# Kernel optimization log

Measured on AMD Instinct MI355X. Metric: run time of the kernel, lower is better.

## Reference

```python
import jax, jax.numpy as jnp
import numpy as np
from jax import lax

B, L, H = 2, 1024, 1024
D = 2048          # intermediate_size
N = 16            # ssm state size
K = 4             # conv kernel
R = 64            # time_step_rank


def setup_inputs() -> dict:
    key = jax.random.key(0)
    ks = jax.random.split(key, 10)
    def nrm(k, shape, scale=0.02):
        return jax.random.normal(k, shape, dtype=jnp.float32) * scale
    A = jnp.arange(1, N + 1, dtype=jnp.float32)[None, :] * jnp.ones((D, 1), jnp.float32)
    return {
        "hidden_states": jax.random.normal(ks[0], (B, L, H), dtype=jnp.float32),
        "W_in":  nrm(ks[1], (2 * D, H)),
        "conv_w": nrm(ks[2], (D, 1, K), 0.1),
        "conv_b": nrm(ks[3], (D,), 0.1),
        "W_x":   nrm(ks[4], (R + 2 * N, D)),
        "W_dt":  nrm(ks[5], (D, R), 0.1),
        "b_dt":  jnp.full((D,), -4.6, jnp.float32),  # softplus(-4.6) ~ 0.01 dt init
        "A_log": jnp.log(A),
        "D_param": jnp.ones((D,), jnp.float32),
        "W_out": nrm(ks[6], (H, D)),
    }


def _mamba_forward(hidden_states, W_in, conv_w, conv_b, W_x, W_dt, b_dt, A_log, D_param, W_out):
    silu = jax.nn.silu
    # in_proj -> [B, L, 2D], chunk into x and gate
    proj = jnp.einsum("blh,eh->ble", hidden_states, W_in)
    x, gate = jnp.split(proj, 2, axis=-1)           # [B,L,D] each
    # depthwise causal conv over time: [B,D,L]
    xc = x.swapaxes(1, 2)
    xc = lax.conv_general_dilated(
        xc, conv_w, window_strides=(1,), padding=[(K - 1, 0)],
        dimension_numbers=("NCH", "OIH", "NCH"), feature_group_count=D)
    x = silu(xc + conv_b[None, :, None]).swapaxes(1, 2)   # [B,L,D]
    # x_proj -> dt, Bmat, Cmat
    ssm_p = jnp.einsum("bld,rd->blr", x, W_x)             # [B,L,R+2N]
    dt_lr, Bm, Cm = ssm_p[..., :R], ssm_p[..., R:R + N], ssm_p[..., R + N:]
    dt = jax.nn.softplus(jnp.einsum("blr,dr->bld", dt_lr, W_dt) + b_dt)  # [B,L,D]
    A = -jnp.exp(A_log)                                   # [D,N]
    dA = jnp.exp(dt[..., None] * A[None, None])           # [B,L,D,N]
    dBu = dt[..., None] * Bm[:, :, None, :] * x[..., None]  # [B,L,D,N]
    # selective scan over time
    def step(h, inp):
        dA_t, dBu_t, C_t = inp                            # [B,D,N],[B,D,N],[B,N]
        h = dA_t * h + dBu_t
        y = jnp.einsum("bdn,bn->bd", h, C_t)
        return h, y
    h0 = jnp.zeros((B, D, N), dt.dtype)
    _, ys = lax.scan(step, h0, (dA.swapaxes(0, 1), dBu.swapaxes(0, 1), Cm.swapaxes(0, 1)))
    y = ys.swapaxes(0, 1)                                 # [B,L,D]
    y = (y + x * D_param[None, None, :]) * silu(gate)
    return jnp.einsum("bld,hd->blh", y, W_out)            # [B,L,H]


def reference(hidden_states, W_in, conv_w, conv_b, W_x, W_dt, b_dt, A_log, D_param, W_out):
    return _mamba_forward(hidden_states, W_in, conv_w, conv_b, W_x, W_dt, b_dt, A_log, D_param, W_out)
```

## Files before the change

kernel.cpp:

```cpp
#include <hip/hip_runtime.h>
#include <hip/hip_bf16.h>
#include <math.h>

#define B_ 2
#define L_ 1024
#define H_ 1024
#define D_ 2048
#define N_ 16
#define R_ 64
#define NCK 32
#define CL 32

typedef short short8 __attribute__((ext_vector_type(8)));
typedef float floatx4 __attribute__((ext_vector_type(4)));

__device__ __forceinline__ float siluf(float g) {
    return g / (1.0f + __expf(-g));
}

__device__ __forceinline__ unsigned short f2bf(float f) {
    unsigned int u = __float_as_uint(f);
    u = (u + 0x7fffu + ((u >> 16) & 1u)) >> 16;
    return (unsigned short)u;
}

__device__ __forceinline__ float bf2f(unsigned short u) {
    return __uint_as_float(((unsigned int)u) << 16);
}

__device__ __forceinline__ void gl2lds(const unsigned short* g, unsigned short* l) {
    __builtin_amdgcn_global_load_lds(
        (const __attribute__((address_space(1))) unsigned int*)g,
        (__attribute__((address_space(3))) unsigned int*)l, 16, 0, 0);
}

#define Q0 524288
#define Q1 1572864
#define Q2 2097152
#define Q3 2146304
#define Q4 2179072
__global__ __launch_bounds__(256) void cvt_all(
    const float* __restrict__ i0, const float* __restrict__ i1,
    const float* __restrict__ i2, const float* __restrict__ i3,
    const float* __restrict__ i4,
    unsigned short* __restrict__ o0, unsigned short* __restrict__ o1,
    unsigned short* __restrict__ o2, unsigned short* __restrict__ o3,
    unsigned short* __restrict__ o4)
{
    int q = blockIdx.x * 256 + threadIdx.x;
    if (q >= Q4) return;
    const float* in; unsigned short* out; int base;
    if (q < Q0)      { in = i0; out = o0; base = 0; }
    else if (q < Q1) { in = i1; out = o1; base = Q0; }
    else if (q < Q2) { in = i2; out = o2; base = Q1; }
    else if (q < Q3) { in = i3; out = o3; base = Q2; }
    else             { in = i4; out = o4; base = Q3; }
    int i = (q - base) * 4;
    float4 v = *(const float4*)(in + i);
    ushort4 o;
    o.x = f2bf(v.x); o.y = f2bf(v.y); o.z = f2bf(v.z); o.w = f2bf(v.w);
    *(ushort4*)(out + i) = o;
}

template<int EPI>
__global__ __launch_bounds__(256) void gemm_bf16_nt(
    const unsigned short* __restrict__ A, const unsigned short* __restrict__ Bm,
    float* __restrict__ C, int K, int Ncols, int ldc, int kChunk, int nMax,
    size_t partStride, float* __restrict__ C2)
{
    __shared__ unsigned short As[2][64 * 32];
    __shared__ unsigned short Bs[2][128 * 32];
    const int tid  = threadIdx.x;
    const int lane = tid & 63;
    const int wave = tid >> 6;
    const int wm = (wave >> 1) * 32;
    const int wn = (wave & 1) * 64;
    const int lr   = lane & 15;
    const int quad = lane >> 4;
    const int m0 = blockIdx.y * 64;
    const int n0 = blockIdx.x * 128;
    const int k0 = blockIdx.z * kChunk;

    const int lrow = lane >> 2;
    const int sq   = (lane & 3) * 8;
    const size_t aoff  = (size_t)(m0 + wave * 16 + lrow) * K + sq;
    const size_t boff0 = (size_t)min(n0 + wave * 32 + lrow, nMax - 1) * K + sq;
    const size_t boff1 = (size_t)min(n0 + wave * 32 + 16 + lrow, nMax - 1) * K + sq;

    floatx4 acc[2][4];
#pragma unroll
    for (int mi = 0; mi < 2; ++mi)
#pragma unroll
        for (int ni = 0; ni < 4; ++ni)
            acc[mi][ni] = (floatx4){0.f, 0.f, 0.f, 0.f};

    gl2lds(A + aoff + k0, &As[0][(wave * 16) * 32]);
    gl2lds(Bm + boff0 + k0, &Bs[0][(wave * 32) * 32]);
    gl2lds(Bm + boff1 + k0, &Bs[0][(wave * 32 + 16) * 32]);

    const int nt = kChunk / 32;
    for (int t = 0; t < nt; ++t) {
        const int cur = t & 1;
        if (t + 1 < nt) {
            const int kt = k0 + (t + 1) * 32;
            gl2lds(A + aoff + kt, &As[cur ^ 1][(wave * 16) * 32]);
            gl2lds(Bm + boff0 + kt, &Bs[cur ^ 1][(wave * 32) * 32]);
            gl2lds(Bm + boff1 + kt, &Bs[cur ^ 1][(wave * 32 + 16) * 32]);
            asm volatile("s_waitcnt vmcnt(3)" ::: "memory");
        } else {
            asm volatile("s_waitcnt vmcnt(0)" ::: "memory");
        }
        __builtin_amdgcn_s_barrier();
        __builtin_amdgcn_sched_barrier(0);

        short8 af[2], bf[4];
#pragma unroll
        for (int mi = 0; mi < 2; ++mi)
            af[mi] = *(const short8*)&As[cur][(wm + mi * 16 + lr) * 32 + quad * 8];
#pragma unroll
        for (int ni = 0; ni < 4; ++ni)
            bf[ni] = *(const short8*)&Bs[cur][(wn + ni * 16 + lr) * 32 + quad * 8];
#pragma unroll
        for (int mi = 0; mi < 2; ++mi)
#pragma unroll
            for (int ni = 0; ni < 4; ++ni)
                acc[mi][ni] = __builtin_amdgcn_mfma_f32_16x16x32_bf16(
                    af[mi], bf[ni], acc[mi][ni], 0, 0, 0);

        asm volatile("s_waitcnt lgkmcnt(0)" ::: "memory");
        __builtin_amdgcn_s_barrier();
    }

    float* Cz = C + (size_t)blockIdx.z * partStride;
#pragma unroll
    for (int mi = 0; mi < 2; ++mi)
#pragma unroll
        for (int ni = 0; ni < 4; ++ni) {
            const int rr = m0 + wm + mi * 16 + quad * 4;
            const int cc = n0 + wn + ni * 16 + lr;
            if (cc >= Ncols) continue;
            if (EPI == 4) {
                if (cc < 2048) {
#pragma unroll
                    for (int r = 0; r < 4; ++r)
                        C[(size_t)(rr + r) * 2048 + cc] = acc[mi][ni][r];
                } else {
#pragma unroll
                    for (int r = 0; r < 4; ++r)
                        C2[(size_t)(rr + r) * 2048 + (cc - 2048)] = acc[mi][ni][r];
                }
            } else {
#pragma unroll
                for (int r = 0; r < 4; ++r)
                    Cz[(size_t)(rr + r) * ldc + cc] = acc[mi][ni][r];
            }
        }
}

__global__ __launch_bounds__(256) void reduce_ssm(
    const float* __restrict__ P, float* __restrict__ ssm_p,
    unsigned short* __restrict__ sp64)
{
    const int q = blockIdx.x * 256 + threadIdx.x;
    const int m = q / 24;
    const int c = (q - m * 24) * 4;
    const size_t idx = (size_t)m * 96 + c;
    float4 s = make_float4(0.f, 0.f, 0.f, 0.f);
#pragma unroll
    for (int z = 0; z < 16; ++z) {
        float4 v = *(const float4*)(P + (size_t)z * (2048 * 96) + idx);
        s.x += v.x; s.y += v.y; s.z += v.z; s.w += v.w;
    }
    *(float4*)(ssm_p + idx) = s;
    if (c < 64) {
        ushort4 o;
        o.x = f2bf(s.x); o.y = f2bf(s.y); o.z = f2bf(s.z); o.w = f2bf(s.w);
        *(ushort4*)(sp64 + (size_t)m * 64 + c) = o;
    }
}

__global__ __launch_bounds__(256) void reduce_out(
    const float* __restrict__ P, float* __restrict__ out)
{
    const size_t i = ((size_t)blockIdx.x * 256 + threadIdx.x) * 4;
    float4 a = *(const float4*)(P + i);
    float4 b = *(const float4*)(P + 2097152 + i);
    float4 c = *(const float4*)(P + 2 * 2097152 + i);
    float4 d = *(const float4*)(P + 3 * 2097152 + i);
    *(float4*)(out + i) = make_float4(a.x + b.x + c.x + d.x,
                                      a.y + b.y + c.y + d.y,
                                      a.z + b.z + c.z + d.z,
                                      a.w + b.w + c.w + d.w);
}

__global__ __launch_bounds__(256) void dt_gemm(
    const unsigned short* __restrict__ A,
    const unsigned short* __restrict__ Bm,
    float* __restrict__ C,
    const float* __restrict__ bias)
{
    __shared__ unsigned short As[64 * 72];
    __shared__ unsigned short Bs[64 * 72];
    const int tid = threadIdx.x;
    const int lane = tid & 63;
    const int wave = tid >> 6;
    const int lr = lane & 15;
    const int quad = lane >> 4;
    const int n0 = blockIdx.x * 64;
    const int m0 = blockIdx.y * 64;

    {
        const int row = tid >> 3;
        const int cq = (tid & 7) * 8;
        uint4 a0 = *(const uint4*)(A + (size_t)(m0 + row) * 64 + cq);
        uint4 a1 = *(const uint4*)(A + (size_t)(m0 + 32 + row) * 64 + cq);
        uint4 b0 = *(const uint4*)(Bm + (size_t)(n0 + row) * 64 + cq);
        uint4 b1 = *(const uint4*)(Bm + (size_t)(n0 + 32 + row) * 64 + cq);
        *(uint4*)&As[row * 72 + cq] = a0;
        *(uint4*)&As[(32 + row) * 72 + cq] = a1;
        *(uint4*)&Bs[row * 72 + cq] = b0;
        *(uint4*)&Bs[(32 + row) * 72 + cq] = b1;
    }
    __syncthreads();

    floatx4 acc[4];
#pragma unroll
    for (int ni = 0; ni < 4; ++ni) acc[ni] = (floatx4){0.f, 0.f, 0.f, 0.f};

#pragma unroll
    for (int kt = 0; kt < 64; kt += 32) {
        short8 af = *(const short8*)&As[(wave * 16 + lr) * 72 + kt + quad * 8];
#pragma unroll
        for (int ni = 0; ni < 4; ++ni) {
            short8 bf = *(const short8*)&Bs[(ni * 16 + lr) * 72 + kt + quad * 8];
            acc[ni] = __builtin_amdgcn_mfma_f32_16x16x32_bf16(af, bf, acc[ni], 0, 0, 0);
        }
    }

    const int rr = m0 + wave * 16 + quad * 4;
#pragma unroll
    for (int ni = 0; ni < 4; ++ni) {
        const int cc = n0 + ni * 16 + lr;
        const float bv = bias[cc];
#pragma unroll
        for (int r = 0; r < 4; ++r) {
            const float z = acc[ni][r] + bv;
            const float spv = fmaxf(z, 0.f) + __logf(1.f + __expf(-fabsf(z)));
            C[(size_t)(rr + r) * 2048 + cc] = spv;
        }
    }
}

__global__ __launch_bounds__(256) void conv_silu_kernel(
    const float* __restrict__ xpre, const float* __restrict__ conv_w,
    const float* __restrict__ conv_b, unsigned short* __restrict__ x_bf)
{
    __shared__ float inT[67][64];
    __shared__ unsigned short tile[64][72];
    const int t = threadIdx.x;
    const int d0 = blockIdx.x * 64;
    const int lt0 = blockIdx.y * 64;
    const int b = blockIdx.z;

    {
        const int r = t >> 2;
        const int q = (t & 3) * 16;
        const int l = lt0 + r - 3;
        if (l >= 0) {
            const float* src = xpre + ((size_t)(b * 1024 + l)) * 2048 + d0 + q;
            *(float4*)&inT[r][q + 0]  = *(const float4*)(src + 0);
            *(float4*)&inT[r][q + 4]  = *(const float4*)(src + 4);
            *(float4*)&inT[r][q + 8]  = *(const float4*)(src + 8);
            *(float4*)&inT[r][q + 12] = *(const float4*)(src + 12);
        } else {
            float4 z4 = make_float4(0.f, 0.f, 0.f, 0.f);
            *(float4*)&inT[r][q + 0]  = z4;
            *(float4*)&inT[r][q + 4]  = z4;
            *(float4*)&inT[r][q + 8]  = z4;
            *(float4*)&inT[r][q + 12] = z4;
        }
        if (t < 12) {
            const int r2 = 64 + (t >> 2);
            const int l2 = lt0 + r2 - 3;
            const float* src = xpre + ((size_t)(b * 1024 + l2)) * 2048 + d0 + q;
            *(float4*)&inT[r2][q + 0]  = *(const float4*)(src + 0);
            *(float4*)&inT[r2][q + 4]  = *(const float4*)(src + 4);
            *(float4*)&inT[r2][q + 8]  = *(const float4*)(src + 8);
            *(float4*)&inT[r2][q + 12] = *(const float4*)(src + 12);
        }
    }
    __syncthreads();

    const int dl = t & 63;
    const int seg = t >> 6;
    const int d = d0 + dl;
    const float w0 = conv_w[d * 4 + 0], w1 = conv_w[d * 4 + 1];
    const float w2 = conv_w[d * 4 + 2], w3 = conv_w[d * 4 + 3];
    const float bias = conv_b[d];

    float p[19];
#pragma unroll
    for (int j = 0; j < 19; ++j) p[j] = inT[seg * 16 + j][dl];
#pragma unroll
    for (int j = 0; j < 16; ++j) {
        float v = siluf(bias + w0 * p[j] + w1 * p[j + 1] + w2 * p[j + 2] + w3 * p[j + 3]);
        tile[seg * 16 + j][dl] = f2bf(v);
    }
    __syncthreads();

    const int ml = t >> 2;
    const int c = t & 3;
    short8 s0 = *(const short8*)&tile[ml][c * 16];
    short8 s1 = *(const short8*)&tile[ml][c * 16 + 8];
    unsigned short* dst = x_bf + (size_t)(b * 1024 + lt0 + ml) * 2048 + d0 + c * 16;
    *(short8*)dst = s0;
    *(short8*)(dst + 8) = s1;
}

__global__ __launch_bounds__(256) void scan_p1(
    const float* __restrict__ dt, const unsigned short* __restrict__ x_bf,
    const float* __restrict__ sp, const float* __restrict__ A_log,
    float* __restrict__ Dts, float* __restrict__ Hch)
{
    __shared__ float sB[CL][16];
    const int tid = threadIdx.x;
    const int d = blockIdx.x * 256 + tid;
    const int ck = blockIdx.y;
    const int b = blockIdx.z;
    const int mb = b * 1024 + ck * CL;

    if (tid < CL * 4) {
        int row = tid >> 2, q = (tid & 3) * 4;
        *(float4*)&sB[row][q] = *(const float4*)(sp + (size_t)(mb + row) * 96 + 64 + q);
    }
    float An2[16];
    {
        const float* al = A_log + d * 16;
#pragma unroll
        for (int j = 0; j < 16; j += 4) {
            float4 a4 = *(const float4*)(al + j);
            An2[j + 0] = -__expf(a4.x) * 1.44269504f;
            An2[j + 1] = -__expf(a4.y) * 1.44269504f;
            An2[j + 2] = -__expf(a4.z) * 1.44269504f;
            An2[j + 3] = -__expf(a4.w) * 1.44269504f;
        }
    }
    __syncthreads();

    float h[16];
#pragma unroll
    for (int n = 0; n < 16; ++n) h[n] = 0.f;
    float dts = 0.f;

    for (int l = 0; l < CL; ++l) {
        const size_t off = (size_t)(mb + l) * 2048 + d;
        const float dtv = dt[off];
        const float xv = bf2f(x_bf[off]);
        const float u = dtv * xv;
        dts += dtv;
        float4 B0 = *(const float4*)&sB[l][0];
        float4 B1 = *(const float4*)&sB[l][4];
        float4 B2 = *(const float4*)&sB[l][8];
        float4 B3 = *(const float4*)&sB[l][12];
        float Bv[16] = {B0.x, B0.y, B0.z, B0.w, B1.x, B1.y, B1.z, B1.w,
                        B2.x, B2.y, B2.z, B2.w, B3.x, B3.y, B3.z, B3.w};
#pragma unroll
        for (int n = 0; n < 16; ++n) {
            const float dA = __builtin_amdgcn_exp2f(dtv * An2[n]);
            h[n] = fmaf(dA, h[n], Bv[n] * u);
        }
    }

    const size_t cb = (size_t)(b * NCK + ck) * 2048 + d;
    Dts[cb] = dts;
    const size_t base = cb * 16;
#pragma unroll
    for (int j = 0; j < 16; j += 4)
        *(float4*)(Hch + base + j) = make_float4(h[j], h[j + 1], h[j + 2], h[j + 3]);
}

__global__ __launch_bounds__(256) void scan_combine(
    const float* __restrict__ Dts, const float* __restrict__ Hch,
    const float* __restrict__ A_log, float* __restrict__ Hin)
{
    const int flat = blockIdx.x * 256 + threadIdx.x;
    const int dn = flat & 32767;
    const int b = flat >> 15;
    const int d = dn >> 4;
    const float An2 = -__expf(A_log[dn]) * 1.44269504f;
    float hin = 0.f;
#pragma unroll 4
    for (int ck = 0; ck < NCK; ++ck) {
        const size_t cb = (size_t)(b * NCK + ck) * 2048 + d;
        const float p = __builtin_amdgcn_exp2f(Dts[cb] * An2);
        const size_t a = ((size_t)(b * NCK + ck) << 15) + dn;
        const float hc = Hch[a];
        Hin[a] = hin;
        hin = fmaf(p, hin, hc);
    }
}

__global__ __launch_bounds__(256) void scan_p2(
    const float* __restrict__ dt, const unsigned short* __restrict__ x_bf,
    const float* __restrict__ gate, const float* __restrict__ sp,
    const float* __restrict__ A_log, const float* __restrict__ Dp,
    const float* __restrict__ Hin, unsigned short* __restrict__ y_bf)
{
    __shared__ float sBC[CL][32];
    const int tid = threadIdx.x;
    const int d = blockIdx.x * 256 + tid;
    const int ck = blockIdx.y;
    const int b = blockIdx.z;
    const int mb = b * 1024 + ck * CL;

    {
        int row = tid >> 3, q = (tid & 7) * 4;
        *(float4*)&sBC[row][q] = *(const float4*)(sp + (size_t)(mb + row) * 96 + 64 + q);
    }
    float An2[16];
    {
        const float* al = A_log + d * 16;
#pragma unroll
        for (int j = 0; j < 16; j += 4) {
            float4 a4 = *(const float4*)(al + j);
            An2[j + 0] = -__expf(a4.x) * 1.44269504f;
            An2[j + 1] = -__expf(a4.y) * 1.44269504f;
            An2[j + 2] = -__expf(a4.z) * 1.44269504f;
            An2[j + 3] = -__expf(a4.w) * 1.44269504f;
        }
    }
    float h[16];
    {
        const size_t base = ((size_t)(b * NCK + ck) * 2048 + d) * 16;
#pragma unroll
        for (int j = 0; j < 16; j += 4) {
            float4 hv = *(const float4*)(Hin + base + j);
            h[j] = hv.x; h[j + 1] = hv.y; h[j + 2] = hv.z; h[j + 3] = hv.w;
        }
    }
    const float Dv = Dp[d];
    __syncthreads();

    for (int l = 0; l < CL; ++l) {
        const size_t off = (size_t)(mb + l) * 2048 + d;
        const float dtv = dt[off];
        const float xv = bf2f(x_bf[off]);
        const float gv = gate[off];
        const float u = dtv * xv;
        float4 B0 = *(const float4*)&sBC[l][0];
        float4 B1 = *(const float4*)&sBC[l][4];
        float4 B2 = *(const float4*)&sBC[l][8];
        float4 B3 = *(const float4*)&sBC[l][12];
        float Bv[16] = {B0.x, B0.y, B0.z, B0.w, B1.x, B1.y, B1.z, B1.w,
                        B2.x, B2.y, B2.z, B2.w, B3.x, B3.y, B3.z, B3.w};
#pragma unroll
        for (int n = 0; n < 16; ++n) {
            const float dA = __builtin_amdgcn_exp2f(dtv * An2[n]);
            h[n] = fmaf(dA, h[n], Bv[n] * u);
        }
        float4 C0 = *(const float4*)&sBC[l][16];
        float4 C1 = *(const float4*)&sBC[l][20];
        float4 C2 = *(const float4*)&sBC[l][24];
        float4 C3 = *(const float4*)&sBC[l][28];
        float Cv[16] = {C0.x, C0.y, C0.z, C0.w, C1.x, C1.y, C1.z, C1.w,
                        C2.x, C2.y, C2.z, C2.w, C3.x, C3.y, C3.z, C3.w};
        float p = 0.f;
#pragma unroll
        for (int n = 0; n < 16; ++n)
            p = fmaf(h[n], Cv[n], p);
        y_bf[off] = f2bf(fmaf(xv, Dv, p) * siluf(gv));
    }
}

extern "C" void kernel_launch(void* const* d_in, const int* in_sizes, int n_in,
                              void* d_out, int out_size, void* d_ws, size_t ws_size,
                              hipStream_t stream)
{
    const float* hs     = (const float*)d_in[0];
    const float* W_in   = (const float*)d_in[1];
    const float* conv_w = (const float*)d_in[2];
    const float* conv_b = (const float*)d_in[3];
    const float* W_x    = (const float*)d_in[4];
    const float* W_dt   = (const float*)d_in[5];
    const float* b_dt   = (const float*)d_in[6];
    const float* A_log  = (const float*)d_in[7];
    const float* Dp     = (const float*)d_in[8];
    const float* W_out  = (const float*)d_in[9];
    float* out = (float*)d_out;

    float* ws    = (float*)d_ws;
    float* gate  = ws;
    float* dtb   = gate + (size_t)4194304;
    float* xpre  = dtb + (size_t)4194304;
    float* ssm_p = xpre + (size_t)4194304;
    unsigned short* hs_bf    = (unsigned short*)(ssm_p + 196608);
    unsigned short* W_in_bf  = hs_bf + (size_t)2097152;
    unsigned short* W_out_bf = W_in_bf + (size_t)4194304;
    unsigned short* W_x_bf   = W_out_bf + (size_t)2097152;
    unsigned short* W_dt_bf  = W_x_bf + (size_t)196608;
    unsigned short* sp64_bf  = W_dt_bf + (size_t)131072;
    unsigned short* x_bf     = sp64_bf + (size_t)131072;
    float* Dts  = (float*)(x_bf + (size_t)4194304);
    float* P1   = xpre;
    float* Hin  = xpre;
    float* Hch  = xpre + (size_t)2097152;
    float* Pout = gate;
    unsigned short* y_bf = hs_bf;

    const int M = B_ * L_;

    cvt_all<<<(Q4 + 255) / 256, 256, 0, stream>>>(
        hs, W_in, W_out, W_x, W_dt, hs_bf, W_in_bf, W_out_bf, W_x_bf, W_dt_bf);

    gemm_bf16_nt<4><<<dim3(4096 / 128, M / 64, 1), 256, 0, stream>>>(
        hs_bf, W_in_bf, xpre, 1024, 4096, 2048, 1024, 4096, 0, gate);

    conv_silu_kernel<<<dim3(D_ / 64, L_ / 64, B_), 256, 0, stream>>>(
        xpre, conv_w, conv_b, x_bf);

    gemm_bf16_nt<0><<<dim3(1, M / 64, 16), 256, 0, stream>>>(
        x_bf, W_x_bf, P1, 2048, 96, 96, 128, 96, (size_t)2048 * 96, nullptr);

    reduce_ssm<<<(2048 * 24) / 256, 256, 0, stream>>>(P1, ssm_p, sp64_bf);

    dt_gemm<<<dim3(2048 / 64, 2048 / 64), 256, 0, stream>>>(
        sp64_bf, W_dt_bf, dtb, b_dt);

    scan_p1<<<dim3(D_ / 256, NCK, B_), 256, 0, stream>>>(
        dtb, x_bf, ssm_p, A_log, Dts, Hch);
    scan_combine<<<(B_ * D_ * 16) / 256, 256, 0, stream>>>(Dts, Hch, A_log, Hin);
    scan_p2<<<dim3(D_ / 256, NCK, B_), 256, 0, stream>>>(
        dtb, x_bf, gate, ssm_p, A_log, Dp, Hin, y_bf);

    gemm_bf16_nt<0><<<dim3(1024 / 128, M / 64, 4), 256, 0, stream>>>(
        y_bf, W_out_bf, Pout, 2048, 1024, 1024, 512, 1024, (size_t)2048 * 1024, nullptr);

    reduce_out<<<(2048 * 1024 / 4) / 256, 256, 0, stream>>>(Pout, out);
}
```

Baseline: 226.8 us.

## Deepen GEMM K-tile to 64 with XOR-swizzled LDS and halve out-proj split-K

```diff
diff --git a/kernel.cpp b/kernel.cpp
--- a/kernel.cpp
+++ b/kernel.cpp
@@ -68,8 +68,8 @@
     float* __restrict__ C, int K, int Ncols, int ldc, int kChunk, int nMax,
     size_t partStride, float* __restrict__ C2)
 {
-    __shared__ unsigned short As[2][64 * 32];
-    __shared__ unsigned short Bs[2][128 * 32];
+    __shared__ unsigned short As[2][64 * 64];
+    __shared__ unsigned short Bs[2][128 * 64];
     const int tid  = threadIdx.x;
     const int lane = tid & 63;
     const int wave = tid >> 6;
@@ -81,11 +81,16 @@
     const int n0 = blockIdx.x * 128;
     const int k0 = blockIdx.z * kChunk;
 
-    const int lrow = lane >> 2;
-    const int sq   = (lane & 3) * 8;
-    const size_t aoff  = (size_t)(m0 + wave * 16 + lrow) * K + sq;
-    const size_t boff0 = (size_t)min(n0 + wave * 32 + lrow, nMax - 1) * K + sq;
-    const size_t boff1 = (size_t)min(n0 + wave * 32 + 16 + lrow, nMax - 1) * K + sq;
+    const int rowIn8 = lane >> 3;
+    const int colSw  = ((lane & 7) ^ rowIn8) * 8;
+    const size_t aoff0 = (size_t)(m0 + 0  + wave * 8 + rowIn8) * K + colSw;
+    const size_t aoff1 = (size_t)(m0 + 32 + wave * 8 + rowIn8) * K + colSw;
+    const size_t boff0 = (size_t)min(n0 + 0  + wave * 8 + rowIn8, nMax - 1) * K + colSw;
+    const size_t boff1 = (size_t)min(n0 + 32 + wave * 8 + rowIn8, nMax - 1) * K + colSw;
+    const size_t boff2 = (size_t)min(n0 + 64 + wave * 8 + rowIn8, nMax - 1) * K + colSw;
+    const size_t boff3 = (size_t)min(n0 + 96 + wave * 8 + rowIn8, nMax - 1) * K + colSw;
+    const int rq0 = ((quad) ^ (lr & 7)) * 8;
+    const int rq1 = rq0 ^ 32;
 
     floatx4 acc[2][4];
 #pragma unroll
@@ -94,42 +99,58 @@
         for (int ni = 0; ni < 4; ++ni)
             acc[mi][ni] = (floatx4){0.f, 0.f, 0.f, 0.f};
 
-    gl2lds(A + aoff + k0, &As[0][(wave * 16) * 32]);
-    gl2lds(Bm + boff0 + k0, &Bs[0][(wave * 32) * 32]);
-    gl2lds(Bm + boff1 + k0, &Bs[0][(wave * 32 + 16) * 32]);
-
-    const int nt = kChunk / 32;
+#define STAGE(buf, kt)                                                   \
+    do {                                                                 \
+        gl2lds(A + aoff0 + (kt), &As[buf][(0  + wave * 8) * 64]);        \
+        gl2lds(A + aoff1 + (kt), &As[buf][(32 + wave * 8) * 64]);        \
+        gl2lds(Bm + boff0 + (kt), &Bs[buf][(0   + wave * 8) * 64]);      \
+        gl2lds(Bm + boff1 + (kt), &Bs[buf][(32  + wave * 8) * 64]);      \
+        gl2lds(Bm + boff2 + (kt), &Bs[buf][(64  + wave * 8) * 64]);      \
+        gl2lds(Bm + boff3 + (kt), &Bs[buf][(96  + wave * 8) * 64]);      \
+    } while (0)
+
+    STAGE(0, k0);
+
+    const int nt = kChunk >> 6;
     for (int t = 0; t < nt; ++t) {
         const int cur = t & 1;
         if (t + 1 < nt) {
-            const int kt = k0 + (t + 1) * 32;
-            gl2lds(A + aoff + kt, &As[cur ^ 1][(wave * 16) * 32]);
-            gl2lds(Bm + boff0 + kt, &Bs[cur ^ 1][(wave * 32) * 32]);
-            gl2lds(Bm + boff1 + kt, &Bs[cur ^ 1][(wave * 32 + 16) * 32]);
-            asm volatile("s_waitcnt vmcnt(3)" ::: "memory");
+            STAGE(cur ^ 1, k0 + (t + 1) * 64);
+            asm volatile("s_waitcnt vmcnt(6)" ::: "memory");
         } else {
             asm volatile("s_waitcnt vmcnt(0)" ::: "memory");
         }
         __builtin_amdgcn_s_barrier();
         __builtin_amdgcn_sched_barrier(0);
 
-        short8 af[2], bf[4];
-#pragma unroll
-        for (int mi = 0; mi < 2; ++mi)
-            af[mi] = *(const short8*)&As[cur][(wm + mi * 16 + lr) * 32 + quad * 8];
-#pragma unroll
-        for (int ni = 0; ni < 4; ++ni)
-            bf[ni] = *(const short8*)&Bs[cur][(wn + ni * 16 + lr) * 32 + quad * 8];
+        short8 a0[2], a1[2], b0[4], b1[4];
+#pragma unroll
+        for (int mi = 0; mi < 2; ++mi) {
+            a0[mi] = *(const short8*)&As[cur][(wm + mi * 16 + lr) * 64 + rq0];
+            a1[mi] = *(const short8*)&As[cur][(wm + mi * 16 + lr) * 64 + rq1];
+        }
+#pragma unroll
+        for (int ni = 0; ni < 4; ++ni) {
+            b0[ni] = *(const short8*)&Bs[cur][(wn + ni * 16 + lr) * 64 + rq0];
+            b1[ni] = *(const short8*)&Bs[cur][(wn + ni * 16 + lr) * 64 + rq1];
+        }
 #pragma unroll
         for (int mi = 0; mi < 2; ++mi)
 #pragma unroll
             for (int ni = 0; ni < 4; ++ni)
                 acc[mi][ni] = __builtin_amdgcn_mfma_f32_16x16x32_bf16(
-                    af[mi], bf[ni], acc[mi][ni], 0, 0, 0);
+                    a0[mi], b0[ni], acc[mi][ni], 0, 0, 0);
+#pragma unroll
+        for (int mi = 0; mi < 2; ++mi)
+#pragma unroll
+            for (int ni = 0; ni < 4; ++ni)
+                acc[mi][ni] = __builtin_amdgcn_mfma_f32_16x16x32_bf16(
+                    a1[mi], b1[ni], acc[mi][ni], 0, 0, 0);
 
         asm volatile("s_waitcnt lgkmcnt(0)" ::: "memory");
         __builtin_amdgcn_s_barrier();
     }
+#undef STAGE
 
     float* Cz = C + (size_t)blockIdx.z * partStride;
 #pragma unroll
@@ -185,12 +206,7 @@
     const size_t i = ((size_t)blockIdx.x * 256 + threadIdx.x) * 4;
     float4 a = *(const float4*)(P + i);
     float4 b = *(const float4*)(P + 2097152 + i);
-    float4 c = *(const float4*)(P + 2 * 2097152 + i);
-    float4 d = *(const float4*)(P + 3 * 2097152 + i);
-    *(float4*)(out + i) = make_float4(a.x + b.x + c.x + d.x,
-                                      a.y + b.y + c.y + d.y,
-                                      a.z + b.z + c.z + d.z,
-                                      a.w + b.w + c.w + d.w);
+    *(float4*)(out + i) = make_float4(a.x + b.x, a.y + b.y, a.z + b.z, a.w + b.w);
 }
 
 __global__ __launch_bounds__(256) void dt_gemm(
@@ -532,8 +548,8 @@
     scan_p2<<<dim3(D_ / 256, NCK, B_), 256, 0, stream>>>(
         dtb, x_bf, gate, ssm_p, A_log, Dp, Hin, y_bf);
 
-    gemm_bf16_nt<0><<<dim3(1024 / 128, M / 64, 4), 256, 0, stream>>>(
-        y_bf, W_out_bf, Pout, 2048, 1024, 1024, 512, 1024, (size_t)2048 * 1024, nullptr);
+    gemm_bf16_nt<0><<<dim3(1024 / 128, M / 64, 2), 256, 0, stream>>>(
+        y_bf, W_out_bf, Pout, 2048, 1024, 1024, 1024, 1024, (size_t)2048 * 1024, nullptr);
 
     reduce_out<<<(2048 * 1024 / 4) / 256, 256, 0, stream>>>(Pout, out);
 }
```

Result: no change. 227.0 us (+0.1%).
